# Kernel optimization log

Hardware: AMD Instinct MI355X
Metric: run time of the kernel (lower is better)

The kernel has to match this reference:

```python
import jax, jax.numpy as jnp
import numpy as np

BATCH, SEQ, DIM = 4, 4096, 1024


def setup_inputs() -> dict:
    key = jax.random.key(0)
    ks = jax.random.split(key, 7)
    return {
        "x": jax.random.normal(ks[0], (BATCH, SEQ, DIM), dtype=jnp.float32),
        "hidden_r": jax.random.normal(ks[1], (BATCH, DIM), dtype=jnp.float32),
        "hidden_i": jax.random.normal(ks[2], (BATCH, DIM), dtype=jnp.float32),
        "phazor_r": jax.random.normal(ks[3], (DIM,), dtype=jnp.float32),
        "phazor_i": jax.random.normal(ks[4], (DIM,), dtype=jnp.float32),
        "phazor_init_r": jax.random.normal(ks[5], (DIM,), dtype=jnp.float32),
        "phazor_init_i": jax.random.normal(ks[6], (DIM,), dtype=jnp.float32),
    }


def reference(x, hidden_r, hidden_i, phazor_r, phazor_i, phazor_init_r, phazor_init_i):
    L = x.shape[1]
    phazor_p = phazor_r + 1j * phazor_i              # raw parameter, (dim,)
    phazor_init = phazor_init_r + 1j * phazor_init_i  # (dim,)
    hidden = hidden_r + 1j * hidden_i                 # (batch, dim)

    mag = jnp.abs(phazor_p)
    phazor = phazor_p / mag * jnp.exp(-mag)           # unit-direction * exp(-|p|), (dim,)

    # (len, dim): phazor ** t for t in [0, len)
    t = jnp.arange(L)[:, None]
    phazor_prog = phazor[None, :] ** t

    filt = phazor_prog * phazor_init[None, :]         # (len, dim)
    filt_fft = jnp.fft.fft(filt, n=2 * L, axis=0)     # (2len, dim)
    x_fft = jnp.fft.fft(x.astype(jnp.complex64), n=2 * L, axis=1)  # (batch, 2len, dim)

    conv = jnp.fft.ifft(filt_fft[None, :, :] * x_fft, axis=1)[:, :L, :]  # (batch, len, dim)

    out = conv + hidden[:, None, :] * phazor_prog[None, :, :] * phazor[None, None, :]
    return out
```

## Files before the change

### kernel.cpp

```cpp
#include <hip/hip_runtime.h>
#include <math.h>

#define BATCH 4
#define SEQ   4096
#define DIM   1024
#define VEC   4

__device__ __forceinline__ void load_params4(
    const float* __restrict__ phr, const float* __restrict__ phi,
    const float* __restrict__ pir, const float* __restrict__ pii,
    int d0, float* ar, float* ai, float* br, float* bi)
{
    float4 p_r = *reinterpret_cast<const float4*>(phr + d0);
    float4 p_i = *reinterpret_cast<const float4*>(phi + d0);
    float4 q_r = *reinterpret_cast<const float4*>(pir + d0);
    float4 q_i = *reinterpret_cast<const float4*>(pii + d0);
    float prv[VEC] = {p_r.x, p_r.y, p_r.z, p_r.w};
    float piv[VEC] = {p_i.x, p_i.y, p_i.z, p_i.w};
    float qrv[VEC] = {q_r.x, q_r.y, q_r.z, q_r.w};
    float qiv[VEC] = {q_i.x, q_i.y, q_i.z, q_i.w};
#pragma unroll
    for (int j = 0; j < VEC; ++j) {
        float mag = sqrtf(prv[j] * prv[j] + piv[j] * piv[j]);
        float s = expf(-mag) / mag;
        ar[j] = prv[j] * s;
        ai[j] = piv[j] * s;
        br[j] = qrv[j];
        bi[j] = qiv[j];
    }
}

template <int NC>
__global__ __launch_bounds__(256) void k_carry(
    const float* __restrict__ x,
    const float* __restrict__ phr, const float* __restrict__ phi,
    const float* __restrict__ pir, const float* __restrict__ pii,
    float2* __restrict__ carry)
{
    constexpr int S = SEQ / NC;
    const int d0 = (blockIdx.x * blockDim.x + threadIdx.x) * VEC;
    const int c = blockIdx.y, b = blockIdx.z;

    float ar[VEC], ai[VEC], br[VEC], bi[VEC];
    load_params4(phr, phi, pir, pii, d0, ar, ai, br, bi);

    const float* xp = x + ((size_t)b * SEQ + (size_t)c * S) * DIM + d0;
    float Cr[VEC] = {0.f, 0.f, 0.f, 0.f};
    float Ci[VEC] = {0.f, 0.f, 0.f, 0.f};
#pragma unroll 4
    for (int t = 0; t < S; ++t) {
        float4 xv = *reinterpret_cast<const float4*>(xp + (size_t)t * DIM);
        float xa[VEC] = {xv.x, xv.y, xv.z, xv.w};
#pragma unroll
        for (int j = 0; j < VEC; ++j) {
            float nr = fmaf(ar[j], Cr[j], fmaf(-ai[j], Ci[j], br[j] * xa[j]));
            float ni = fmaf(ar[j], Ci[j], fmaf( ai[j], Cr[j], bi[j] * xa[j]));
            Cr[j] = nr; Ci[j] = ni;
        }
    }
    float2* cp = carry + ((size_t)b * NC + c) * DIM + d0;
#pragma unroll
    for (int j = 0; j < VEC; ++j) cp[j] = make_float2(Cr[j], Ci[j]);
}

template <int NC>
__global__ __launch_bounds__(256) void k_prefix(
    const float* __restrict__ phr, const float* __restrict__ phi,
    const float* __restrict__ hr,  const float* __restrict__ hi_,
    const float2* __restrict__ carry,
    float2* __restrict__ prefix)
{
    constexpr int S = SEQ / NC;
    const int idx = blockIdx.x * blockDim.x + threadIdx.x;
    const int b = idx / DIM, d = idx % DIM;

    float pr = phr[d], pi = phi[d];
    float mag = sqrtf(pr * pr + pi * pi);
    float sc = expf(-mag) / mag;
    float ar = pr * sc, ai = pi * sc;

    float Ar = 1.f, Ai = 0.f, sr = ar, si = ai;
    int e = S;
    while (e) {
        if (e & 1) {
            float nr = Ar * sr - Ai * si;
            Ai = Ar * si + Ai * sr;
            Ar = nr;
        }
        float nr = sr * sr - si * si;
        si = 2.f * sr * si;
        sr = nr;
        e >>= 1;
    }

    float2 cv[NC];
#pragma unroll
    for (int c = 0; c < NC; ++c)
        cv[c] = carry[((size_t)b * NC + c) * DIM + d];

    float Pr = hr[idx], Pi = hi_[idx];
#pragma unroll
    for (int c = 0; c < NC; ++c) {
        prefix[((size_t)b * NC + c) * DIM + d] = make_float2(Pr, Pi);
        float nr = fmaf(Ar, Pr, fmaf(-Ai, Pi, cv[c].x));
        float ni = fmaf(Ar, Pi, fmaf( Ai, Pr, cv[c].y));
        Pr = nr; Pi = ni;
    }
}

template <int NC, bool CPLX>
__global__ __launch_bounds__(256) void k_out(
    const float* __restrict__ x,
    const float* __restrict__ phr, const float* __restrict__ phi,
    const float* __restrict__ pir, const float* __restrict__ pii,
    const float2* __restrict__ prefix,
    float* __restrict__ out)
{
    constexpr int S = SEQ / NC;
    const int d0 = (blockIdx.x * blockDim.x + threadIdx.x) * VEC;
    const int c = blockIdx.y, b = blockIdx.z;

    float ar[VEC], ai[VEC], br[VEC], bi[VEC];
    load_params4(phr, phi, pir, pii, d0, ar, ai, br, bi);

    float Cr[VEC], Ci[VEC];
    const float2* pp = prefix + ((size_t)b * NC + c) * DIM + d0;
#pragma unroll
    for (int j = 0; j < VEC; ++j) {
        float2 v = pp[j];
        Cr[j] = v.x; Ci[j] = v.y;
    }

    const float* xp = x + ((size_t)b * SEQ + (size_t)c * S) * DIM + d0;
    const size_t obase = ((size_t)b * SEQ + (size_t)c * S) * DIM + d0;
#pragma unroll 2
    for (int t = 0; t < S; ++t) {
        float4 xv = *reinterpret_cast<const float4*>(xp + (size_t)t * DIM);
        float xa[VEC] = {xv.x, xv.y, xv.z, xv.w};
#pragma unroll
        for (int j = 0; j < VEC; ++j) {
            float nr = fmaf(ar[j], Cr[j], fmaf(-ai[j], Ci[j], br[j] * xa[j]));
            float ni = fmaf(ar[j], Ci[j], fmaf( ai[j], Cr[j], bi[j] * xa[j]));
            Cr[j] = nr; Ci[j] = ni;
        }
        if (CPLX) {
            float4* dst = reinterpret_cast<float4*>(out + 2 * (obase + (size_t)t * DIM));
            dst[0] = make_float4(Cr[0], Ci[0], Cr[1], Ci[1]);
            dst[1] = make_float4(Cr[2], Ci[2], Cr[3], Ci[3]);
        } else {
            *reinterpret_cast<float4*>(out + obase + (size_t)t * DIM) =
                make_float4(Cr[0], Cr[1], Cr[2], Cr[3]);
        }
    }
}

template <bool CPLX>
__global__ void k_serial(
    const float* __restrict__ x,
    const float* __restrict__ phr, const float* __restrict__ phi,
    const float* __restrict__ pir, const float* __restrict__ pii,
    const float* __restrict__ hr,  const float* __restrict__ hi_,
    float* __restrict__ out)
{
    const int idx = blockIdx.x * blockDim.x + threadIdx.x;
    if (idx >= BATCH * DIM) return;
    const int b = idx / DIM, d = idx % DIM;

    float pr = phr[d], pi = phi[d];
    float mag = sqrtf(pr * pr + pi * pi);
    float sc = expf(-mag) / mag;
    float ar = pr * sc, ai = pi * sc;
    float br = pir[d], bi = pii[d];

    float Cr = hr[idx], Ci = hi_[idx];
    const float* xp = x + (size_t)b * SEQ * DIM + d;
    for (int t = 0; t < SEQ; ++t) {
        float xv = xp[(size_t)t * DIM];
        float nr = fmaf(ar, Cr, fmaf(-ai, Ci, br * xv));
        float ni = fmaf(ar, Ci, fmaf( ai, Cr, bi * xv));
        Cr = nr; Ci = ni;
        size_t o = ((size_t)b * SEQ + t) * DIM + d;
        if (CPLX) {
            reinterpret_cast<float2*>(out)[o] = make_float2(Cr, Ci);
        } else {
            out[o] = Cr;
        }
    }
}

template <int NC, bool CPLX>
static void run_all(const float* x, const float* hr, const float* hi_,
                    const float* phr, const float* phi,
                    const float* pir, const float* pii,
                    float* out, void* d_ws, hipStream_t stream)
{
    float2* carry = (float2*)d_ws;
    float2* prefix = carry + (size_t)BATCH * NC * DIM;

    dim3 blk(256);
    dim3 g1(DIM / (256 * VEC), NC, BATCH);
    k_carry<NC><<<g1, blk, 0, stream>>>(x, phr, phi, pir, pii, carry);
    k_prefix<NC><<<dim3(BATCH * DIM / 256), blk, 0, stream>>>(
        phr, phi, hr, hi_, carry, prefix);
    k_out<NC, CPLX><<<g1, blk, 0, stream>>>(x, phr, phi, pir, pii, prefix, out);
}

template <bool CPLX>
static void dispatch(const float* x, const float* hr, const float* hi_,
                     const float* phr, const float* phi,
                     const float* pir, const float* pii,
                     float* out, void* d_ws, size_t ws_size, hipStream_t stream)
{
    auto need = [](int nc) { return (size_t)2 * BATCH * nc * DIM * sizeof(float2); };

    if (ws_size >= need(64))
        run_all<64, CPLX>(x, hr, hi_, phr, phi, pir, pii, out, d_ws, stream);
    else if (ws_size >= need(32))
        run_all<32, CPLX>(x, hr, hi_, phr, phi, pir, pii, out, d_ws, stream);
    else if (ws_size >= need(16))
        run_all<16, CPLX>(x, hr, hi_, phr, phi, pir, pii, out, d_ws, stream);
    else
        k_serial<CPLX><<<dim3((BATCH * DIM + 255) / 256), dim3(256), 0, stream>>>(
            x, phr, phi, pir, pii, hr, hi_, out);
}

extern "C" void kernel_launch(void* const* d_in, const int* in_sizes, int n_in,
                              void* d_out, int out_size, void* d_ws, size_t ws_size,
                              hipStream_t stream) {
    const float* x   = (const float*)d_in[0];
    const float* hr  = (const float*)d_in[1];
    const float* hi_ = (const float*)d_in[2];
    const float* phr = (const float*)d_in[3];
    const float* phi = (const float*)d_in[4];
    const float* pir = (const float*)d_in[5];
    const float* pii = (const float*)d_in[6];
    float* out = (float*)d_out;

    const size_t total = (size_t)BATCH * SEQ * DIM;
    if ((size_t)out_size >= 2 * total)
        dispatch<true >(x, hr, hi_, phr, phi, pir, pii, out, d_ws, ws_size, stream);
    else
        dispatch<false>(x, hr, hi_, phr, phi, pir, pii, out, d_ws, ws_size, stream);
}
```

Measured before the change: 146.8 us.

## Parallelize chunk-prefix with wave-level scan and raise chunk count

Replaces the per-(batch,dim) serial prefix over chunk carries with a 64-lane wavefront scan of affine complex maps using shuffles, one wave per (batch,dim). This allows many more chunks (up to 256) so the carry and output kernels expose more parallelism and shorter serial loops per thread. The cost is more prefix-kernel threads and shuffle work, plus a larger workspace requirement. Removing the NC=16/32 fallbacks means small workspaces now drop straight to the slow serial kernel.

```diff
diff --git a/kernel.cpp b/kernel.cpp
--- a/kernel.cpp
+++ b/kernel.cpp
@@ -64,46 +64,73 @@
 }
 
 template <int NC>
-__global__ __launch_bounds__(256) void k_prefix(
+__global__ __launch_bounds__(256) void k_prefix_wave(
     const float* __restrict__ phr, const float* __restrict__ phi,
     const float* __restrict__ hr,  const float* __restrict__ hi_,
     const float2* __restrict__ carry,
     float2* __restrict__ prefix)
 {
     constexpr int S = SEQ / NC;
-    const int idx = blockIdx.x * blockDim.x + threadIdx.x;
-    const int b = idx / DIM, d = idx % DIM;
+    constexpr int CPL = NC / 64;
+    const int wave = (blockIdx.x * blockDim.x + threadIdx.x) >> 6;
+    const int lane = threadIdx.x & 63;
+    const int b = wave / DIM, d = wave % DIM;
 
     float pr = phr[d], pi = phi[d];
     float mag = sqrtf(pr * pr + pi * pi);
     float sc = expf(-mag) / mag;
     float ar = pr * sc, ai = pi * sc;
-
     float Ar = 1.f, Ai = 0.f, sr = ar, si = ai;
     int e = S;
     while (e) {
-        if (e & 1) {
-            float nr = Ar * sr - Ai * si;
-            Ai = Ar * si + Ai * sr;
-            Ar = nr;
-        }
-        float nr = sr * sr - si * si;
-        si = 2.f * sr * si;
-        sr = nr;
+        if (e & 1) { float nr = Ar * sr - Ai * si; Ai = Ar * si + Ai * sr; Ar = nr; }
+        float nr = sr * sr - si * si; si = 2.f * sr * si; sr = nr;
         e >>= 1;
     }
 
-    float2 cv[NC];
-#pragma unroll
-    for (int c = 0; c < NC; ++c)
-        cv[c] = carry[((size_t)b * NC + c) * DIM + d];
-
-    float Pr = hr[idx], Pi = hi_[idx];
-#pragma unroll
-    for (int c = 0; c < NC; ++c) {
-        prefix[((size_t)b * NC + c) * DIM + d] = make_float2(Pr, Pi);
-        float nr = fmaf(Ar, Pr, fmaf(-Ai, Pi, cv[c].x));
-        float ni = fmaf(Ar, Pi, fmaf( Ai, Pr, cv[c].y));
+    float2 cv[CPL];
+#pragma unroll
+    for (int j = 0; j < CPL; ++j)
+        cv[j] = carry[((size_t)b * NC + lane * CPL + j) * DIM + d];
+
+    float mr = 1.f, mi = 0.f, rr = 0.f, ri = 0.f;
+#pragma unroll
+    for (int j = 0; j < CPL; ++j) {
+        float nmr = Ar * mr - Ai * mi;
+        float nmi = Ar * mi + Ai * mr;
+        float nrr = fmaf(Ar, rr, fmaf(-Ai, ri, cv[j].x));
+        float nri = fmaf(Ar, ri, fmaf( Ai, rr, cv[j].y));
+        mr = nmr; mi = nmi; rr = nrr; ri = nri;
+    }
+
+#pragma unroll
+    for (int off = 1; off < 64; off <<= 1) {
+        float pmr = __shfl_up(mr, off);
+        float pmi = __shfl_up(mi, off);
+        float prr = __shfl_up(rr, off);
+        float pri = __shfl_up(ri, off);
+        if (lane >= off) {
+            float nmr = mr * pmr - mi * pmi;
+            float nmi = mr * pmi + mi * pmr;
+            float nrr = fmaf(mr, prr, fmaf(-mi, pri, rr));
+            float nri = fmaf(mr, pri, fmaf( mi, prr, ri));
+            mr = nmr; mi = nmi; rr = nrr; ri = nri;
+        }
+    }
+    float emr = __shfl_up(mr, 1);
+    float emi = __shfl_up(mi, 1);
+    float err_ = __shfl_up(rr, 1);
+    float eri = __shfl_up(ri, 1);
+    if (lane == 0) { emr = 1.f; emi = 0.f; err_ = 0.f; eri = 0.f; }
+
+    float h_r = hr[wave], h_i = hi_[wave];
+    float Pr = fmaf(emr, h_r, fmaf(-emi, h_i, err_));
+    float Pi = fmaf(emr, h_i, fmaf( emi, h_r, eri));
+#pragma unroll
+    for (int j = 0; j < CPL; ++j) {
+        prefix[((size_t)b * NC + lane * CPL + j) * DIM + d] = make_float2(Pr, Pi);
+        float nr = fmaf(Ar, Pr, fmaf(-Ai, Pi, cv[j].x));
+        float ni = fmaf(Ar, Pi, fmaf( Ai, Pr, cv[j].y));
         Pr = nr; Pi = ni;
     }
 }
@@ -200,7 +227,7 @@
     dim3 blk(256);
     dim3 g1(DIM / (256 * VEC), NC, BATCH);
     k_carry<NC><<<g1, blk, 0, stream>>>(x, phr, phi, pir, pii, carry);
-    k_prefix<NC><<<dim3(BATCH * DIM / 256), blk, 0, stream>>>(
+    k_prefix_wave<NC><<<dim3(BATCH * DIM * 64 / 256), blk, 0, stream>>>(
         phr, phi, hr, hi_, carry, prefix);
     k_out<NC, CPLX><<<g1, blk, 0, stream>>>(x, phr, phi, pir, pii, prefix, out);
 }
@@ -213,12 +240,12 @@
 {
     auto need = [](int nc) { return (size_t)2 * BATCH * nc * DIM * sizeof(float2); };
 
-    if (ws_size >= need(64))
+    if (ws_size >= need(256))
+        run_all<256, CPLX>(x, hr, hi_, phr, phi, pir, pii, out, d_ws, stream);
+    else if (ws_size >= need(128))
+        run_all<128, CPLX>(x, hr, hi_, phr, phi, pir, pii, out, d_ws, stream);
+    else if (ws_size >= need(64))
         run_all<64, CPLX>(x, hr, hi_, phr, phi, pir, pii, out, d_ws, stream);
-    else if (ws_size >= need(32))
-        run_all<32, CPLX>(x, hr, hi_, phr, phi, pir, pii, out, d_ws, stream);
-    else if (ws_size >= need(16))
-        run_all<16, CPLX>(x, hr, hi_, phr, phi, pir, pii, out, d_ws, stream);
     else
         k_serial<CPLX><<<dim3((BATCH * DIM + 255) / 256), dim3(256), 0, stream>>>(
             x, phr, phi, pir, pii, hr, hi_, out);
```

Measured after the change: 150.0 us. +2.2%, slower.

## Fuse chunked scan into single kernel with decoupled look-back prefix propagation

Applied to the files above, without the earlier changes.

Replaces the three-kernel carry/prefix/output pipeline with one kernel. Each block computes its chunk aggregate, publishes it, then resolves its incoming prefix with a decoupled look-back over earlier chunks' published aggregates and inclusive prefixes. It then reruns the recurrence to write outputs and publishes its own inclusive prefix. The goal is to avoid two extra launches and the carry/prefix round trips, and the chunk count rises so more blocks run. The cost is a workspace memset, spin-waiting on global atomics, and reliance on blocks being scheduled in increasing index order to avoid deadlock. x is still read twice.

```diff
diff --git a/kernel.cpp b/kernel.cpp
--- a/kernel.cpp
+++ b/kernel.cpp
@@ -5,6 +5,19 @@
 #define SEQ   4096
 #define DIM   1024
 #define VEC   4
+
+#define SENT 0xFFFFFFFFFFFFFFFFull
+
+static __device__ __forceinline__ unsigned long long pack2(float r, float i) {
+    union { float2 f; unsigned long long u; } v;
+    v.f = make_float2(r, i);
+    return v.u;
+}
+static __device__ __forceinline__ float2 unpack2(unsigned long long u) {
+    union { float2 f; unsigned long long u; } v;
+    v.u = u;
+    return v.f;
+}
 
 __device__ __forceinline__ void load_params4(
     const float* __restrict__ phr, const float* __restrict__ phi,
@@ -30,16 +43,20 @@
     }
 }
 
-template <int NC>
-__global__ __launch_bounds__(256) void k_carry(
+template <int NC, bool CPLX>
+__global__ __launch_bounds__(256, 4) void k_fused(
     const float* __restrict__ x,
     const float* __restrict__ phr, const float* __restrict__ phi,
     const float* __restrict__ pir, const float* __restrict__ pii,
-    float2* __restrict__ carry)
+    const float* __restrict__ hr,  const float* __restrict__ hi_,
+    unsigned long long* __restrict__ agg,
+    unsigned long long* __restrict__ pre,
+    float* __restrict__ out)
 {
     constexpr int S = SEQ / NC;
-    const int d0 = (blockIdx.x * blockDim.x + threadIdx.x) * VEC;
-    const int c = blockIdx.y, b = blockIdx.z;
+    const int bid = blockIdx.x;
+    const int c = bid / BATCH, b = bid % BATCH;
+    const int d0 = threadIdx.x * VEC;
 
     float ar[VEC], ai[VEC], br[VEC], bi[VEC];
     load_params4(phr, phi, pir, pii, d0, ar, ai, br, bi);
@@ -58,80 +75,86 @@
             Cr[j] = nr; Ci[j] = ni;
         }
     }
-    float2* cp = carry + ((size_t)b * NC + c) * DIM + d0;
-#pragma unroll
-    for (int j = 0; j < VEC; ++j) cp[j] = make_float2(Cr[j], Ci[j]);
-}
-
-template <int NC>
-__global__ __launch_bounds__(256) void k_prefix(
-    const float* __restrict__ phr, const float* __restrict__ phi,
-    const float* __restrict__ hr,  const float* __restrict__ hi_,
-    const float2* __restrict__ carry,
-    float2* __restrict__ prefix)
-{
-    constexpr int S = SEQ / NC;
-    const int idx = blockIdx.x * blockDim.x + threadIdx.x;
-    const int b = idx / DIM, d = idx % DIM;
-
-    float pr = phr[d], pi = phi[d];
-    float mag = sqrtf(pr * pr + pi * pi);
-    float sc = expf(-mag) / mag;
-    float ar = pr * sc, ai = pi * sc;
-
-    float Ar = 1.f, Ai = 0.f, sr = ar, si = ai;
-    int e = S;
-    while (e) {
-        if (e & 1) {
-            float nr = Ar * sr - Ai * si;
-            Ai = Ar * si + Ai * sr;
-            Ar = nr;
-        }
-        float nr = sr * sr - si * si;
-        si = 2.f * sr * si;
-        sr = nr;
-        e >>= 1;
-    }
-
-    float2 cv[NC];
-#pragma unroll
-    for (int c = 0; c < NC; ++c)
-        cv[c] = carry[((size_t)b * NC + c) * DIM + d];
-
-    float Pr = hr[idx], Pi = hi_[idx];
-#pragma unroll
-    for (int c = 0; c < NC; ++c) {
-        prefix[((size_t)b * NC + c) * DIM + d] = make_float2(Pr, Pi);
-        float nr = fmaf(Ar, Pr, fmaf(-Ai, Pi, cv[c].x));
-        float ni = fmaf(Ar, Pi, fmaf( Ai, Pr, cv[c].y));
-        Pr = nr; Pi = ni;
-    }
-}
-
-template <int NC, bool CPLX>
-__global__ __launch_bounds__(256) void k_out(
-    const float* __restrict__ x,
-    const float* __restrict__ phr, const float* __restrict__ phi,
-    const float* __restrict__ pir, const float* __restrict__ pii,
-    const float2* __restrict__ prefix,
-    float* __restrict__ out)
-{
-    constexpr int S = SEQ / NC;
-    const int d0 = (blockIdx.x * blockDim.x + threadIdx.x) * VEC;
-    const int c = blockIdx.y, b = blockIdx.z;
-
-    float ar[VEC], ai[VEC], br[VEC], bi[VEC];
-    load_params4(phr, phi, pir, pii, d0, ar, ai, br, bi);
-
-    float Cr[VEC], Ci[VEC];
-    const float2* pp = prefix + ((size_t)b * NC + c) * DIM + d0;
+
+    const size_t lbase = ((size_t)b * NC + c) * DIM + d0;
+#pragma unroll
+    for (int j = 0; j < VEC; ++j)
+        __hip_atomic_store(&agg[lbase + j], pack2(Cr[j], Ci[j]),
+                           __ATOMIC_RELAXED, __HIP_MEMORY_SCOPE_AGENT);
+
+    float Ar[VEC], Ai[VEC];
 #pragma unroll
     for (int j = 0; j < VEC; ++j) {
-        float2 v = pp[j];
-        Cr[j] = v.x; Ci[j] = v.y;
-    }
-
-    const float* xp = x + ((size_t)b * SEQ + (size_t)c * S) * DIM + d0;
+        float mr = 1.f, mi = 0.f, sr = ar[j], si = ai[j];
+        int e = S;
+        while (e) {
+            if (e & 1) { float nr = mr * sr - mi * si; mi = mr * si + mi * sr; mr = nr; }
+            float nr = sr * sr - si * si; si = 2.f * sr * si; sr = nr;
+            e >>= 1;
+        }
+        Ar[j] = mr; Ai[j] = mi;
+    }
+
+    float Pr[VEC], Pi[VEC];
+    if (c == 0) {
+#pragma unroll
+        for (int j = 0; j < VEC; ++j) {
+            Pr[j] = hr[b * DIM + d0 + j];
+            Pi[j] = hi_[b * DIM + d0 + j];
+        }
+    } else {
+        float aR[VEC] = {0.f,0.f,0.f,0.f}, aI[VEC] = {0.f,0.f,0.f,0.f};
+        float WR[VEC] = {1.f,1.f,1.f,1.f}, WI[VEC] = {0.f,0.f,0.f,0.f};
+        int j = c - 1;
+        for (;;) {
+            const size_t pbase = ((size_t)b * NC + j) * DIM + d0;
+            unsigned long long pv[VEC];
+            bool got = true;
+#pragma unroll
+            for (int jj = 0; jj < VEC; ++jj) {
+                pv[jj] = __hip_atomic_load(&pre[pbase + jj],
+                                           __ATOMIC_RELAXED, __HIP_MEMORY_SCOPE_AGENT);
+                got = got && (pv[jj] != SENT);
+            }
+            if (got) {
+#pragma unroll
+                for (int jj = 0; jj < VEC; ++jj) {
+                    float2 v = unpack2(pv[jj]);
+                    Pr[jj] = aR[jj] + WR[jj] * v.x - WI[jj] * v.y;
+                    Pi[jj] = aI[jj] + WR[jj] * v.y + WI[jj] * v.x;
+                }
+                break;
+            }
+#pragma unroll
+            for (int jj = 0; jj < VEC; ++jj) {
+                unsigned long long av;
+                do {
+                    av = __hip_atomic_load(&agg[pbase + jj],
+                                           __ATOMIC_RELAXED, __HIP_MEMORY_SCOPE_AGENT);
+                } while (av == SENT);
+                float2 L = unpack2(av);
+                aR[jj] += WR[jj] * L.x - WI[jj] * L.y;
+                aI[jj] += WR[jj] * L.y + WI[jj] * L.x;
+                float nWR = WR[jj] * Ar[jj] - WI[jj] * Ai[jj];
+                WI[jj] = WR[jj] * Ai[jj] + WI[jj] * Ar[jj];
+                WR[jj] = nWR;
+            }
+            if (--j < 0) {
+#pragma unroll
+                for (int jj = 0; jj < VEC; ++jj) {
+                    float h_r = hr[b * DIM + d0 + jj];
+                    float h_i = hi_[b * DIM + d0 + jj];
+                    Pr[jj] = aR[jj] + WR[jj] * h_r - WI[jj] * h_i;
+                    Pi[jj] = aI[jj] + WR[jj] * h_i + WI[jj] * h_r;
+                }
+                break;
+            }
+        }
+    }
+
+#pragma unroll
+    for (int j = 0; j < VEC; ++j) { Cr[j] = Pr[j]; Ci[j] = Pi[j]; }
+
     const size_t obase = ((size_t)b * SEQ + (size_t)c * S) * DIM + d0;
 #pragma unroll 2
     for (int t = 0; t < S; ++t) {
@@ -151,6 +174,13 @@
             *reinterpret_cast<float4*>(out + obase + (size_t)t * DIM) =
                 make_float4(Cr[0], Cr[1], Cr[2], Cr[3]);
         }
+    }
+
+    if (c < NC - 1) {
+#pragma unroll
+        for (int j = 0; j < VEC; ++j)
+            __hip_atomic_store(&pre[lbase + j], pack2(Cr[j], Ci[j]),
+                               __ATOMIC_RELAXED, __HIP_MEMORY_SCOPE_AGENT);
     }
 }
 
@@ -189,20 +219,17 @@
 }
 
 template <int NC, bool CPLX>
-static void run_all(const float* x, const float* hr, const float* hi_,
-                    const float* phr, const float* phi,
-                    const float* pir, const float* pii,
-                    float* out, void* d_ws, hipStream_t stream)
-{
-    float2* carry = (float2*)d_ws;
-    float2* prefix = carry + (size_t)BATCH * NC * DIM;
-
-    dim3 blk(256);
-    dim3 g1(DIM / (256 * VEC), NC, BATCH);
-    k_carry<NC><<<g1, blk, 0, stream>>>(x, phr, phi, pir, pii, carry);
-    k_prefix<NC><<<dim3(BATCH * DIM / 256), blk, 0, stream>>>(
-        phr, phi, hr, hi_, carry, prefix);
-    k_out<NC, CPLX><<<g1, blk, 0, stream>>>(x, phr, phi, pir, pii, prefix, out);
+static void run_fused(const float* x, const float* hr, const float* hi_,
+                      const float* phr, const float* phi,
+                      const float* pir, const float* pii,
+                      float* out, void* d_ws, hipStream_t stream)
+{
+    const size_t n = (size_t)BATCH * NC * DIM;
+    unsigned long long* agg = (unsigned long long*)d_ws;
+    unsigned long long* pre = agg + n;
+    hipMemsetAsync(d_ws, 0xFF, 2 * n * sizeof(unsigned long long), stream);
+    k_fused<NC, CPLX><<<dim3(NC * BATCH), dim3(256), 0, stream>>>(
+        x, phr, phi, pir, pii, hr, hi_, agg, pre, out);
 }
 
 template <bool CPLX>
@@ -211,14 +238,15 @@
                      const float* pir, const float* pii,
                      float* out, void* d_ws, size_t ws_size, hipStream_t stream)
 {
-    auto need = [](int nc) { return (size_t)2 * BATCH * nc * DIM * sizeof(float2); };
-
-    if (ws_size >= need(64))
-        run_all<64, CPLX>(x, hr, hi_, phr, phi, pir, pii, out, d_ws, stream);
-    else if (ws_size >= need(32))
-        run_all<32, CPLX>(x, hr, hi_, phr, phi, pir, pii, out, d_ws, stream);
-    else if (ws_size >= need(16))
-        run_all<16, CPLX>(x, hr, hi_, phr, phi, pir, pii, out, d_ws, stream);
+    auto need = [](int nc) {
+        return (size_t)2 * BATCH * nc * DIM * sizeof(unsigned long long);
+    };
+    if (ws_size >= need(256))
+        run_fused<256, CPLX>(x, hr, hi_, phr, phi, pir, pii, out, d_ws, stream);
+    else if (ws_size >= need(128))
+        run_fused<128, CPLX>(x, hr, hi_, phr, phi, pir, pii, out, d_ws, stream);
+    else if (ws_size >= need(64))
+        run_fused<64, CPLX>(x, hr, hi_, phr, phi, pir, pii, out, d_ws, stream);
     else
         k_serial<CPLX><<<dim3((BATCH * DIM + 255) / 256), dim3(256), 0, stream>>>(
             x, phr, phi, pir, pii, hr, hi_, out);
```

Result: slower. 207.4 us (+41.3%).

## Fuse prefix scan into output kernel, raise chunk count, use nontemporal memory ops

Applied to the files above, without the earlier changes.

Removes the separate prefix kernel. Each output block now recomputes its own incoming state by summing all earlier chunk carries, weighted by powers of phazor^S. The chunk count rises to 128, giving the carry and output kernels more blocks to fill the GPU. Loads of x and stores of the output use nontemporal hints to reduce cache pollution. In exchange, later chunks do a redundant O(c) carry reduction, which adds up to 127 sequential complex steps per thread, and the fused fast path requires a fixed workspace size.

```diff
diff --git a/kernel.cpp b/kernel.cpp
--- a/kernel.cpp
+++ b/kernel.cpp
@@ -5,6 +5,16 @@
 #define SEQ   4096
 #define DIM   1024
 #define VEC   4
+#define NCC   128
+
+typedef float vfloat4 __attribute__((ext_vector_type(4)));
+
+__device__ __forceinline__ vfloat4 ntload4(const float* p) {
+    return __builtin_nontemporal_load(reinterpret_cast<const vfloat4*>(p));
+}
+__device__ __forceinline__ void ntstore4(float* p, vfloat4 v) {
+    __builtin_nontemporal_store(v, reinterpret_cast<vfloat4*>(p));
+}
 
 __device__ __forceinline__ void load_params4(
     const float* __restrict__ phr, const float* __restrict__ phi,
@@ -30,26 +40,36 @@
     }
 }
 
-template <int NC>
+__device__ __forceinline__ void pow_c(float a_r, float a_i, int e,
+                                      float* outR, float* outI)
+{
+    float Ar = 1.f, Ai = 0.f, sr = a_r, si = a_i;
+    while (e) {
+        if (e & 1) { float nr = Ar * sr - Ai * si; Ai = Ar * si + Ai * sr; Ar = nr; }
+        float nr = sr * sr - si * si; si = 2.f * sr * si; sr = nr;
+        e >>= 1;
+    }
+    *outR = Ar; *outI = Ai;
+}
+
 __global__ __launch_bounds__(256) void k_carry(
     const float* __restrict__ x,
     const float* __restrict__ phr, const float* __restrict__ phi,
     const float* __restrict__ pir, const float* __restrict__ pii,
     float2* __restrict__ carry)
 {
-    constexpr int S = SEQ / NC;
-    const int d0 = (blockIdx.x * blockDim.x + threadIdx.x) * VEC;
+    constexpr int S = SEQ / NCC;
+    const int d0 = threadIdx.x * VEC;
     const int c = blockIdx.y, b = blockIdx.z;
 
     float ar[VEC], ai[VEC], br[VEC], bi[VEC];
     load_params4(phr, phi, pir, pii, d0, ar, ai, br, bi);
 
     const float* xp = x + ((size_t)b * SEQ + (size_t)c * S) * DIM + d0;
-    float Cr[VEC] = {0.f, 0.f, 0.f, 0.f};
-    float Ci[VEC] = {0.f, 0.f, 0.f, 0.f};
+    float Cr[VEC] = {0.f,0.f,0.f,0.f}, Ci[VEC] = {0.f,0.f,0.f,0.f};
 #pragma unroll 4
     for (int t = 0; t < S; ++t) {
-        float4 xv = *reinterpret_cast<const float4*>(xp + (size_t)t * DIM);
+        vfloat4 xv = ntload4(xp + (size_t)t * DIM);
         float xa[VEC] = {xv.x, xv.y, xv.z, xv.w};
 #pragma unroll
         for (int j = 0; j < VEC; ++j) {
@@ -58,98 +78,94 @@
             Cr[j] = nr; Ci[j] = ni;
         }
     }
-    float2* cp = carry + ((size_t)b * NC + c) * DIM + d0;
-#pragma unroll
-    for (int j = 0; j < VEC; ++j) cp[j] = make_float2(Cr[j], Ci[j]);
-}
-
-template <int NC>
-__global__ __launch_bounds__(256) void k_prefix(
-    const float* __restrict__ phr, const float* __restrict__ phi,
+    float4* cp4 = reinterpret_cast<float4*>(carry + ((size_t)b * NCC + c) * DIM + d0);
+    cp4[0] = make_float4(Cr[0], Ci[0], Cr[1], Ci[1]);
+    cp4[1] = make_float4(Cr[2], Ci[2], Cr[3], Ci[3]);
+}
+
+template <bool CPLX>
+__global__ __launch_bounds__(256) void k_out2(
+    const float* __restrict__ x,
+    const float* __restrict__ phr, const float* __restrict__ phi,
+    const float* __restrict__ pir, const float* __restrict__ pii,
     const float* __restrict__ hr,  const float* __restrict__ hi_,
     const float2* __restrict__ carry,
-    float2* __restrict__ prefix)
-{
-    constexpr int S = SEQ / NC;
-    const int idx = blockIdx.x * blockDim.x + threadIdx.x;
-    const int b = idx / DIM, d = idx % DIM;
-
-    float pr = phr[d], pi = phi[d];
-    float mag = sqrtf(pr * pr + pi * pi);
-    float sc = expf(-mag) / mag;
-    float ar = pr * sc, ai = pi * sc;
-
-    float Ar = 1.f, Ai = 0.f, sr = ar, si = ai;
-    int e = S;
-    while (e) {
-        if (e & 1) {
-            float nr = Ar * sr - Ai * si;
-            Ai = Ar * si + Ai * sr;
-            Ar = nr;
-        }
-        float nr = sr * sr - si * si;
-        si = 2.f * sr * si;
-        sr = nr;
-        e >>= 1;
-    }
-
-    float2 cv[NC];
-#pragma unroll
-    for (int c = 0; c < NC; ++c)
-        cv[c] = carry[((size_t)b * NC + c) * DIM + d];
-
-    float Pr = hr[idx], Pi = hi_[idx];
-#pragma unroll
-    for (int c = 0; c < NC; ++c) {
-        prefix[((size_t)b * NC + c) * DIM + d] = make_float2(Pr, Pi);
-        float nr = fmaf(Ar, Pr, fmaf(-Ai, Pi, cv[c].x));
-        float ni = fmaf(Ar, Pi, fmaf( Ai, Pr, cv[c].y));
-        Pr = nr; Pi = ni;
-    }
-}
-
-template <int NC, bool CPLX>
-__global__ __launch_bounds__(256) void k_out(
-    const float* __restrict__ x,
-    const float* __restrict__ phr, const float* __restrict__ phi,
-    const float* __restrict__ pir, const float* __restrict__ pii,
-    const float2* __restrict__ prefix,
     float* __restrict__ out)
 {
-    constexpr int S = SEQ / NC;
-    const int d0 = (blockIdx.x * blockDim.x + threadIdx.x) * VEC;
+    constexpr int S = SEQ / NCC;
+    const int d0 = threadIdx.x * VEC;
     const int c = blockIdx.y, b = blockIdx.z;
 
     float ar[VEC], ai[VEC], br[VEC], bi[VEC];
     load_params4(phr, phi, pir, pii, d0, ar, ai, br, bi);
 
+    float Ar[VEC], Ai[VEC];
+#pragma unroll
+    for (int j = 0; j < VEC; ++j) pow_c(ar[j], ai[j], S, &Ar[j], &Ai[j]);
+
+    float aR[VEC] = {0.f,0.f,0.f,0.f}, aI[VEC] = {0.f,0.f,0.f,0.f};
+    float WR[VEC] = {1.f,1.f,1.f,1.f}, WI[VEC] = {0.f,0.f,0.f,0.f};
+    int j = c - 1;
+    while (j >= 0) {
+        const int g = (j >= 7) ? 8 : (j + 1);
+        float4 buf[8][2];
+#pragma unroll
+        for (int k = 0; k < 8; ++k) {
+            if (k < g) {
+                const float4* cp4 = reinterpret_cast<const float4*>(
+                    carry + ((size_t)b * NCC + (j - k)) * DIM + d0);
+                buf[k][0] = cp4[0];
+                buf[k][1] = cp4[1];
+            }
+        }
+#pragma unroll
+        for (int k = 0; k < 8; ++k) {
+            if (k < g) {
+                float cr[VEC] = {buf[k][0].x, buf[k][0].z, buf[k][1].x, buf[k][1].z};
+                float ci[VEC] = {buf[k][0].y, buf[k][0].w, buf[k][1].y, buf[k][1].w};
+#pragma unroll
+                for (int jj = 0; jj < VEC; ++jj) {
+                    aR[jj] += WR[jj] * cr[jj] - WI[jj] * ci[jj];
+                    aI[jj] += WR[jj] * ci[jj] + WI[jj] * cr[jj];
+                    float nWR = WR[jj] * Ar[jj] - WI[jj] * Ai[jj];
+                    WI[jj] = WR[jj] * Ai[jj] + WI[jj] * Ar[jj];
+                    WR[jj] = nWR;
+                }
+            }
+        }
+        j -= g;
+    }
+
     float Cr[VEC], Ci[VEC];
-    const float2* pp = prefix + ((size_t)b * NC + c) * DIM + d0;
-#pragma unroll
-    for (int j = 0; j < VEC; ++j) {
-        float2 v = pp[j];
-        Cr[j] = v.x; Ci[j] = v.y;
+#pragma unroll
+    for (int jj = 0; jj < VEC; ++jj) {
+        float h_r = hr[b * DIM + d0 + jj];
+        float h_i = hi_[b * DIM + d0 + jj];
+        Cr[jj] = aR[jj] + WR[jj] * h_r - WI[jj] * h_i;
+        Ci[jj] = aI[jj] + WR[jj] * h_i + WI[jj] * h_r;
     }
 
     const float* xp = x + ((size_t)b * SEQ + (size_t)c * S) * DIM + d0;
     const size_t obase = ((size_t)b * SEQ + (size_t)c * S) * DIM + d0;
 #pragma unroll 2
     for (int t = 0; t < S; ++t) {
-        float4 xv = *reinterpret_cast<const float4*>(xp + (size_t)t * DIM);
+        vfloat4 xv = ntload4(xp + (size_t)t * DIM);
         float xa[VEC] = {xv.x, xv.y, xv.z, xv.w};
 #pragma unroll
-        for (int j = 0; j < VEC; ++j) {
-            float nr = fmaf(ar[j], Cr[j], fmaf(-ai[j], Ci[j], br[j] * xa[j]));
-            float ni = fmaf(ar[j], Ci[j], fmaf( ai[j], Cr[j], bi[j] * xa[j]));
-            Cr[j] = nr; Ci[j] = ni;
+        for (int jj = 0; jj < VEC; ++jj) {
+            float nr = fmaf(ar[jj], Cr[jj], fmaf(-ai[jj], Ci[jj], br[jj] * xa[jj]));
+            float ni = fmaf(ar[jj], Ci[jj], fmaf( ai[jj], Cr[jj], bi[jj] * xa[jj]));
+            Cr[jj] = nr; Ci[jj] = ni;
         }
         if (CPLX) {
-            float4* dst = reinterpret_cast<float4*>(out + 2 * (obase + (size_t)t * DIM));
-            dst[0] = make_float4(Cr[0], Ci[0], Cr[1], Ci[1]);
-            dst[1] = make_float4(Cr[2], Ci[2], Cr[3], Ci[3]);
+            float* dst = out + 2 * (obase + (size_t)t * DIM);
+            vfloat4 o0 = {Cr[0], Ci[0], Cr[1], Ci[1]};
+            vfloat4 o1 = {Cr[2], Ci[2], Cr[3], Ci[3]};
+            ntstore4(dst,     o0);
+            ntstore4(dst + 4, o1);
         } else {
-            *reinterpret_cast<float4*>(out + obase + (size_t)t * DIM) =
-                make_float4(Cr[0], Cr[1], Cr[2], Cr[3]);
+            vfloat4 o0 = {Cr[0], Cr[1], Cr[2], Cr[3]};
+            ntstore4(out + obase + (size_t)t * DIM, o0);
         }
     }
 }
@@ -180,29 +196,9 @@
         float ni = fmaf(ar, Ci, fmaf( ai, Cr, bi * xv));
         Cr = nr; Ci = ni;
         size_t o = ((size_t)b * SEQ + t) * DIM + d;
-        if (CPLX) {
-            reinterpret_cast<float2*>(out)[o] = make_float2(Cr, Ci);
-        } else {
-            out[o] = Cr;
-        }
-    }
-}
-
-template <int NC, bool CPLX>
-static void run_all(const float* x, const float* hr, const float* hi_,
-                    const float* phr, const float* phi,
-                    const float* pir, const float* pii,
-                    float* out, void* d_ws, hipStream_t stream)
-{
-    float2* carry = (float2*)d_ws;
-    float2* prefix = carry + (size_t)BATCH * NC * DIM;
-
-    dim3 blk(256);
-    dim3 g1(DIM / (256 * VEC), NC, BATCH);
-    k_carry<NC><<<g1, blk, 0, stream>>>(x, phr, phi, pir, pii, carry);
-    k_prefix<NC><<<dim3(BATCH * DIM / 256), blk, 0, stream>>>(
-        phr, phi, hr, hi_, carry, prefix);
-    k_out<NC, CPLX><<<g1, blk, 0, stream>>>(x, phr, phi, pir, pii, prefix, out);
+        if (CPLX) reinterpret_cast<float2*>(out)[o] = make_float2(Cr, Ci);
+        else      out[o] = Cr;
+    }
 }
 
 template <bool CPLX>
@@ -211,17 +207,19 @@
                      const float* pir, const float* pii,
                      float* out, void* d_ws, size_t ws_size, hipStream_t stream)
 {
-    auto need = [](int nc) { return (size_t)2 * BATCH * nc * DIM * sizeof(float2); };
-
-    if (ws_size >= need(64))
-        run_all<64, CPLX>(x, hr, hi_, phr, phi, pir, pii, out, d_ws, stream);
-    else if (ws_size >= need(32))
-        run_all<32, CPLX>(x, hr, hi_, phr, phi, pir, pii, out, d_ws, stream);
-    else if (ws_size >= need(16))
-        run_all<16, CPLX>(x, hr, hi_, phr, phi, pir, pii, out, d_ws, stream);
-    else
+    const size_t need = (size_t)BATCH * NCC * DIM * sizeof(float2);
+    if (ws_size < need) {
         k_serial<CPLX><<<dim3((BATCH * DIM + 255) / 256), dim3(256), 0, stream>>>(
             x, phr, phi, pir, pii, hr, hi_, out);
+        return;
+    }
+    float2* carry = (float2*)d_ws;
+
+    dim3 blk(256);
+    dim3 g1(1, NCC, BATCH);
+    k_carry<<<g1, blk, 0, stream>>>(x, phr, phi, pir, pii, carry);
+    k_out2<CPLX><<<g1, blk, 0, stream>>>(x, phr, phi, pir, pii, hr, hi_,
+                                         carry, out);
 }
 
 extern "C" void kernel_launch(void* const* d_in, const int* in_sizes, int n_in,
```

After: 174.8 us. 19.1% more time.
